# Performance work log

Hardware: AMD Instinct MI355X
Metric: run time of the kernel (lower is better)

Reference implementation:

```python
import jax, jax.numpy as jnp
import numpy as np

N, NA, F = 16384, 256, 2048
GAMMA = 1.5
BN_EPS = 1e-5


def setup_inputs() -> dict:
    key = jax.random.key(0)
    k1, k2, k3, k4, k5 = jax.random.split(key, 5)
    a = jax.random.normal(k1, (N, NA), dtype=jnp.float32)
    ps = jax.random.uniform(k2, (N, F), dtype=jnp.float32)
    lim = 1.0 / np.sqrt(NA)
    W = jax.random.uniform(k3, (F, NA), minval=-lim, maxval=lim, dtype=jnp.float32)
    b = jax.random.uniform(k4, (F,), minval=-lim, maxval=lim, dtype=jnp.float32)
    bn_w = jnp.ones((F,), dtype=jnp.float32)
    bn_b = jnp.zeros((F,), dtype=jnp.float32)
    return {"a": a, "ps": ps, "W": W, "b": b, "bn_w": bn_w, "bn_b": bn_b}


def sparsemax(z):
    # Faithful translation of the repo's Sparsemax (note: it sorts ASCENDING,
    # exactly as the original torch code does).
    D = z.shape[-1]
    s = jnp.sort(z, axis=-1)                      # ascending, [N, D]
    r = jnp.arange(D, dtype=z.dtype)              # [D]
    w = (1.0 + r * s - jnp.cumsum(s, axis=-1) > 0).astype(jnp.int32)
    k_z = jnp.max(jnp.arange(D, dtype=jnp.int32) * w, axis=-1)   # [N]
    m = (jnp.arange(D)[None, :] < (k_z + 1)[:, None]).astype(z.dtype)  # [N, D]
    m_z = jnp.sum(m * s, axis=-1)                 # [N]
    tau_z = (m_z + 1.0) / k_z.astype(z.dtype)     # [N]
    return jnp.maximum(z - tau_z[:, None], 0.0)


def reference(a, ps, W, b, bn_w, bn_b):
    # Linear: (N, n_a) -> (N, F)
    x = a @ W.T + b
    # BatchNorm1d (training mode: batch statistics, biased variance)
    mu = jnp.mean(x, axis=0)
    var = jnp.mean((x - mu) ** 2, axis=0)
    x = (x - mu) / jnp.sqrt(var + BN_EPS) * bn_w + bn_b
    # Sparsemax over prior-scaled activations
    m = sparsemax(x * ps)
    new_ps = ps * (GAMMA - jax.lax.stop_gradient(m))
    return m, new_ps
```

## Files before the change

### kernel.cpp

```cpp
#include <hip/hip_runtime.h>
#include <hip/hip_bf16.h>
#include <math.h>

#define N_ROWS 16384
#define N_A    256
#define N_F    2048
#define GAMMA  1.5f
#define BN_EPS 1e-5f

typedef __attribute__((ext_vector_type(8))) short short8;
typedef __attribute__((ext_vector_type(4))) float f32x4;

__global__ __launch_bounds__(256) void cvt_bf16(const float* __restrict__ in,
                                                unsigned short* __restrict__ out,
                                                int n4) {
    int i = blockIdx.x * 256 + threadIdx.x;
    if (i >= n4) return;
    float4 v = reinterpret_cast<const float4*>(in)[i];
    ushort4 o;
    o.x = __builtin_bit_cast(unsigned short, __float2bfloat16(v.x));
    o.y = __builtin_bit_cast(unsigned short, __float2bfloat16(v.y));
    o.z = __builtin_bit_cast(unsigned short, __float2bfloat16(v.z));
    o.w = __builtin_bit_cast(unsigned short, __float2bfloat16(v.w));
    reinterpret_cast<ushort4*>(out)[i] = o;
}

__global__ __launch_bounds__(256) void gemm_x(const unsigned short* __restrict__ aB,
                                              const unsigned short* __restrict__ wB,
                                              const float* __restrict__ bias,
                                              unsigned short* __restrict__ xB,
                                              float* __restrict__ ps1,
                                              float* __restrict__ ps2) {
    const int tid  = threadIdx.x;
    const int lane = tid & 63;
    const int wave = tid >> 6;
    const int r16  = lane & 15;
    const int quad = lane >> 4;
    const int col0 = blockIdx.x * 128;
    const int rowB = blockIdx.y * 128;
    const int row0 = rowB + wave * 32;

    __shared__ char smem[65536];

    {
        const char* wsrc = (const char*)(wB + (size_t)col0 * N_A);
        #pragma unroll
        for (int i = 0; i < 16; ++i) {
            const int c   = i * 256 + tid;
            const int row = c >> 5;
            const int off = (c & 31) * 16;
            const int src = off ^ ((row & 7) << 4);
            __builtin_amdgcn_global_load_lds(
                (const __attribute__((address_space(1))) void*)(wsrc + (size_t)row * 512 + src),
                (__attribute__((address_space(3))) void*)(smem + c * 16),
                16, 0, 0);
        }
    }

    f32x4 acc[2][8];
    #pragma unroll
    for (int g = 0; g < 2; ++g)
        #pragma unroll
        for (int t = 0; t < 8; ++t)
            acc[g][t] = (f32x4){0.f, 0.f, 0.f, 0.f};

    const unsigned short* aR0 = aB + (size_t)(row0 + r16) * N_A;
    const unsigned short* aR1 = aR0 + 16 * N_A;

    __syncthreads();

    const int swz = (r16 & 7) << 4;
    #pragma unroll
    for (int ks = 0; ks < 8; ++ks) {
        const int k0  = ks * 32 + quad * 8;
        short8 a0 = *reinterpret_cast<const short8*>(aR0 + k0);
        short8 a1 = *reinterpret_cast<const short8*>(aR1 + k0);
        const int wof = (ks * 64 + quad * 16) ^ swz;
        #pragma unroll
        for (int t = 0; t < 8; ++t) {
            short8 bf = *reinterpret_cast<const short8*>(
                            smem + (t * 16 + r16) * 512 + wof);
            acc[0][t] = __builtin_amdgcn_mfma_f32_16x16x32_bf16(a0, bf, acc[0][t], 0, 0, 0);
            acc[1][t] = __builtin_amdgcn_mfma_f32_16x16x32_bf16(a1, bf, acc[1][t], 0, 0, 0);
        }
    }

    __syncthreads();

    __shared__ float cs1[4][128];
    __shared__ float cs2[4][128];
    unsigned short (*tile)[136] = (unsigned short (*)[136])smem;

    #pragma unroll
    for (int t = 0; t < 8; ++t) {
        const float bcol = bias[col0 + t * 16 + r16];
        float s1 = 0.f, s2 = 0.f;
        #pragma unroll
        for (int g = 0; g < 2; ++g) {
            #pragma unroll
            for (int r = 0; r < 4; ++r) {
                float v = acc[g][t][r] + bcol;
                s1 += v;
                s2 += v * v;
                tile[wave * 32 + g * 16 + quad * 4 + r][t * 16 + r16] =
                    __builtin_bit_cast(unsigned short, __float2bfloat16(v));
            }
        }
        s1 += __shfl_xor(s1, 16); s1 += __shfl_xor(s1, 32);
        s2 += __shfl_xor(s2, 16); s2 += __shfl_xor(s2, 32);
        if (quad == 0) { cs1[wave][t * 16 + r16] = s1; cs2[wave][t * 16 + r16] = s2; }
    }
    __syncthreads();

    if (threadIdx.x < 128) {
        const int c = threadIdx.x;
        float s1 = cs1[0][c] + cs1[1][c] + cs1[2][c] + cs1[3][c];
        float s2 = cs2[0][c] + cs2[1][c] + cs2[2][c] + cs2[3][c];
        ps1[(size_t)blockIdx.y * N_F + col0 + c] = s1;
        ps2[(size_t)blockIdx.y * N_F + col0 + c] = s2;
    }

    {
        const int r = threadIdx.x >> 1;
        const int h = threadIdx.x & 1;
        const unsigned short* src = &tile[r][h * 64];
        unsigned short* dst = xB + (size_t)(rowB + r) * 4096 + col0 + h * 64;
        #pragma unroll
        for (int i = 0; i < 8; ++i)
            *reinterpret_cast<short8*>(dst + i * 8) =
                *reinterpret_cast<const short8*>(src + i * 8);
    }
}

__global__ __launch_bounds__(256) void finalize_stats(const float* __restrict__ ps1,
                                                      const float* __restrict__ ps2,
                                                      const float* __restrict__ bn_w,
                                                      const float* __restrict__ bn_b,
                                                      float* __restrict__ scale,
                                                      float* __restrict__ shift) {
    const int f = blockIdx.x * 256 + threadIdx.x;
    float s1 = 0.f, s2 = 0.f;
    #pragma unroll 4
    for (int i = 0; i < 128; ++i) {
        s1 += ps1[(size_t)i * N_F + f];
        s2 += ps2[(size_t)i * N_F + f];
    }
    const float inv_n = 1.0f / (float)N_ROWS;
    const float mu  = s1 * inv_n;
    const float var = s2 * inv_n - mu * mu;
    const float sc  = bn_w[f] / sqrtf(var + BN_EPS);
    scale[f] = sc;
    shift[f] = bn_b[f] - mu * sc;
}

__global__ __launch_bounds__(256) void bn_sparsemax(const unsigned short* xB,
                                                    const float* __restrict__ ps,
                                                    const float* __restrict__ scale,
                                                    const float* __restrict__ shift,
                                                    float* m_out,
                                                    float* __restrict__ ps_out) {
    const int row = blockIdx.x;
    const int tid = threadIdx.x;
    const int f0  = tid * 8;

    const unsigned short* xr = xB + (size_t)row * 4096 + f0;
    const float* pr = ps + (size_t)row * N_F + f0;

    short8 xv = *reinterpret_cast<const short8*>(xr);
    float4 p0  = *reinterpret_cast<const float4*>(pr);
    float4 p1  = *reinterpret_cast<const float4*>(pr + 4);
    float4 sc0 = *reinterpret_cast<const float4*>(scale + f0);
    float4 sc1 = *reinterpret_cast<const float4*>(scale + f0 + 4);
    float4 sh0 = *reinterpret_cast<const float4*>(shift + f0);
    float4 sh1 = *reinterpret_cast<const float4*>(shift + f0 + 4);

    float pv[8]  = {p0.x, p0.y, p0.z, p0.w, p1.x, p1.y, p1.z, p1.w};
    float scv[8] = {sc0.x, sc0.y, sc0.z, sc0.w, sc1.x, sc1.y, sc1.z, sc1.w};
    float shv[8] = {sh0.x, sh0.y, sh0.z, sh0.w, sh1.x, sh1.y, sh1.z, sh1.w};

    float z[8];
    float s = 0.f, mx = -INFINITY, mn = INFINITY;
    #pragma unroll
    for (int i = 0; i < 8; ++i) {
        float xf = __builtin_bit_cast(float,
                       (unsigned int)((unsigned short)xv[i]) << 16);
        float zz = (xf * scv[i] + shv[i]) * pv[i];
        z[i] = zz;
        s += zz;
        mx = fmaxf(mx, zz);
        mn = fminf(mn, zz);
    }

    #pragma unroll
    for (int off = 32; off > 0; off >>= 1) {
        s  += __shfl_xor(s, off);
        mx  = fmaxf(mx, __shfl_xor(mx, off));
        mn  = fminf(mn, __shfl_xor(mn, off));
    }
    __shared__ float rs[4], rmx[4], rmn[4];
    const int wave = tid >> 6;
    if ((tid & 63) == 0) { rs[wave] = s; rmx[wave] = mx; rmn[wave] = mn; }
    __syncthreads();
    s  = rs[0] + rs[1] + rs[2] + rs[3];
    mx = fmaxf(fmaxf(rmx[0], rmx[1]), fmaxf(rmx[2], rmx[3]));
    mn = fminf(fminf(rmn[0], rmn[1]), fminf(rmn[2], rmn[3]));

    const float c_last = 1.0f + (float)(N_F - 1) * mx - s;
    float tau;
    if (c_last > 0.0f) {
        tau = (s + 1.0f) / (float)(N_F - 1);
    } else {
        tau = (mn + 1.0f) / 0.0f;
    }

    float* mo = m_out  + (size_t)row * N_F + f0;
    float* po = ps_out + (size_t)row * N_F + f0;
    float4 mv0, mv1, po0, po1;
    mv0.x = fmaxf(z[0] - tau, 0.f); po0.x = pv[0] * (GAMMA - mv0.x);
    mv0.y = fmaxf(z[1] - tau, 0.f); po0.y = pv[1] * (GAMMA - mv0.y);
    mv0.z = fmaxf(z[2] - tau, 0.f); po0.z = pv[2] * (GAMMA - mv0.z);
    mv0.w = fmaxf(z[3] - tau, 0.f); po0.w = pv[3] * (GAMMA - mv0.w);
    mv1.x = fmaxf(z[4] - tau, 0.f); po1.x = pv[4] * (GAMMA - mv1.x);
    mv1.y = fmaxf(z[5] - tau, 0.f); po1.y = pv[5] * (GAMMA - mv1.y);
    mv1.z = fmaxf(z[6] - tau, 0.f); po1.z = pv[6] * (GAMMA - mv1.z);
    mv1.w = fmaxf(z[7] - tau, 0.f); po1.w = pv[7] * (GAMMA - mv1.w);
    *reinterpret_cast<float4*>(mo)     = mv0;
    *reinterpret_cast<float4*>(mo + 4) = mv1;
    *reinterpret_cast<float4*>(po)     = po0;
    *reinterpret_cast<float4*>(po + 4) = po1;
}

extern "C" void kernel_launch(void* const* d_in, const int* in_sizes, int n_in,
                              void* d_out, int out_size, void* d_ws, size_t ws_size,
                              hipStream_t stream) {
    const float* a    = (const float*)d_in[0];
    const float* ps   = (const float*)d_in[1];
    const float* W    = (const float*)d_in[2];
    const float* bias = (const float*)d_in[3];
    const float* bnw  = (const float*)d_in[4];
    const float* bnb  = (const float*)d_in[5];

    float* out    = (float*)d_out;
    float* m_out  = out;
    float* ps_out = out + (size_t)N_ROWS * N_F;
    unsigned short* xB = (unsigned short*)d_out;

    char* ws = (char*)d_ws;
    unsigned short* aB = (unsigned short*)ws;
    unsigned short* wB = (unsigned short*)(ws + (8u << 20));
    float* ps1   = (float*)(ws + (9u  << 20));
    float* ps2   = (float*)(ws + (10u << 20));
    float* scale = (float*)(ws + (11u << 20));
    float* shift = (float*)(ws + (11u << 20) + 8192);

    cvt_bf16<<<4096, 256, 0, stream>>>(a, aB, N_ROWS * N_A / 4);
    cvt_bf16<<<512, 256, 0, stream>>>(W, wB, N_F * N_A / 4);
    gemm_x<<<dim3(N_F / 128, N_ROWS / 128), 256, 0, stream>>>(aB, wB, bias, xB, ps1, ps2);
    finalize_stats<<<N_F / 256, 256, 0, stream>>>(ps1, ps2, bnw, bnb, scale, shift);
    bn_sparsemax<<<N_ROWS, 256, 0, stream>>>(xB, ps, scale, shift, m_out, ps_out);
}
```

Measured before the change: 447.6 us.

## Double-buffer GEMM K-slabs in LDS, remap blocks, one-wave-per-row sparsemax

The GEMM now stages both A and W in 64-element K slabs through LDS with double buffering, overlapping the global-to-LDS loads with MFMA work. Previously only W went through LDS and A was read straight from global memory. Block IDs are remapped so that neighbouring blocks share tiles and get better cache locality. The sparsemax kernel now gives each row to a single wave, removing the LDS reduction and __syncthreads, and it re-reads ps in the output phase rather than holding it in registers.

```diff
diff --git a/kernel.cpp b/kernel.cpp
--- a/kernel.cpp
+++ b/kernel.cpp
@@ -36,26 +36,35 @@
     const int wave = tid >> 6;
     const int r16  = lane & 15;
     const int quad = lane >> 4;
-    const int col0 = blockIdx.x * 128;
-    const int rowB = blockIdx.y * 128;
-    const int row0 = rowB + wave * 32;
+
+    const int id   = blockIdx.y * 16 + blockIdx.x;
+    const int nid  = (id & 7) * 256 + (id >> 3);
+    const int bx   = nid & 15;
+    const int by   = nid >> 4;
+    const int col0 = bx * 128;
+    const int rowB = by * 128;
 
     __shared__ char smem[65536];
-
-    {
-        const char* wsrc = (const char*)(wB + (size_t)col0 * N_A);
-        #pragma unroll
-        for (int i = 0; i < 16; ++i) {
+    char* As = smem;
+    char* Ws = smem + 32768;
+
+    auto STAGE = [&](int bo, int slab) {
+        const char* asrc = (const char*)(aB + (size_t)rowB * N_A + slab * 64);
+        const char* wsrc = (const char*)(wB + (size_t)col0 * N_A + slab * 64);
+        #pragma unroll
+        for (int i = 0; i < 4; ++i) {
             const int c   = i * 256 + tid;
-            const int row = c >> 5;
-            const int off = (c & 31) * 16;
+            const int row = c >> 3;
+            const int off = (c & 7) * 16;
             const int src = off ^ ((row & 7) << 4);
             __builtin_amdgcn_global_load_lds(
+                (const __attribute__((address_space(1))) void*)(asrc + (size_t)row * 512 + src),
+                (__attribute__((address_space(3))) void*)(As + bo + c * 16), 16, 0, 0);
+            __builtin_amdgcn_global_load_lds(
                 (const __attribute__((address_space(1))) void*)(wsrc + (size_t)row * 512 + src),
-                (__attribute__((address_space(3))) void*)(smem + c * 16),
-                16, 0, 0);
-        }
-    }
+                (__attribute__((address_space(3))) void*)(Ws + bo + c * 16), 16, 0, 0);
+        }
+    };
 
     f32x4 acc[2][8];
     #pragma unroll
@@ -64,28 +73,31 @@
         for (int t = 0; t < 8; ++t)
             acc[g][t] = (f32x4){0.f, 0.f, 0.f, 0.f};
 
-    const unsigned short* aR0 = aB + (size_t)(row0 + r16) * N_A;
-    const unsigned short* aR1 = aR0 + 16 * N_A;
-
+    STAGE(0, 0);
     __syncthreads();
 
     const int swz = (r16 & 7) << 4;
     #pragma unroll
-    for (int ks = 0; ks < 8; ++ks) {
-        const int k0  = ks * 32 + quad * 8;
-        short8 a0 = *reinterpret_cast<const short8*>(aR0 + k0);
-        short8 a1 = *reinterpret_cast<const short8*>(aR1 + k0);
-        const int wof = (ks * 64 + quad * 16) ^ swz;
-        #pragma unroll
-        for (int t = 0; t < 8; ++t) {
-            short8 bf = *reinterpret_cast<const short8*>(
-                            smem + (t * 16 + r16) * 512 + wof);
-            acc[0][t] = __builtin_amdgcn_mfma_f32_16x16x32_bf16(a0, bf, acc[0][t], 0, 0, 0);
-            acc[1][t] = __builtin_amdgcn_mfma_f32_16x16x32_bf16(a1, bf, acc[1][t], 0, 0, 0);
-        }
-    }
-
-    __syncthreads();
+    for (int s = 0; s < 4; ++s) {
+        const int bo = (s & 1) * 16384;
+        if (s < 3) STAGE(bo ^ 16384, s + 1);
+        #pragma unroll
+        for (int ks = 0; ks < 2; ++ks) {
+            const int koff = (ks * 64 + quad * 16) ^ swz;
+            short8 a0 = *reinterpret_cast<const short8*>(
+                            As + bo + (wave * 32 + r16) * 128 + koff);
+            short8 a1 = *reinterpret_cast<const short8*>(
+                            As + bo + (wave * 32 + 16 + r16) * 128 + koff);
+            #pragma unroll
+            for (int t = 0; t < 8; ++t) {
+                short8 bf = *reinterpret_cast<const short8*>(
+                                Ws + bo + (t * 16 + r16) * 128 + koff);
+                acc[0][t] = __builtin_amdgcn_mfma_f32_16x16x32_bf16(a0, bf, acc[0][t], 0, 0, 0);
+                acc[1][t] = __builtin_amdgcn_mfma_f32_16x16x32_bf16(a1, bf, acc[1][t], 0, 0, 0);
+            }
+        }
+        __syncthreads();
+    }
 
     __shared__ float cs1[4][128];
     __shared__ float cs2[4][128];
@@ -116,8 +128,8 @@
         const int c = threadIdx.x;
         float s1 = cs1[0][c] + cs1[1][c] + cs1[2][c] + cs1[3][c];
         float s2 = cs2[0][c] + cs2[1][c] + cs2[2][c] + cs2[3][c];
-        ps1[(size_t)blockIdx.y * N_F + col0 + c] = s1;
-        ps2[(size_t)blockIdx.y * N_F + col0 + c] = s2;
+        ps1[(size_t)by * N_F + col0 + c] = s1;
+        ps2[(size_t)by * N_F + col0 + c] = s2;
     }
 
     {
@@ -159,36 +171,38 @@
                                                     const float* __restrict__ shift,
                                                     float* m_out,
                                                     float* __restrict__ ps_out) {
-    const int row = blockIdx.x;
-    const int tid = threadIdx.x;
-    const int f0  = tid * 8;
-
-    const unsigned short* xr = xB + (size_t)row * 4096 + f0;
-    const float* pr = ps + (size_t)row * N_F + f0;
-
-    short8 xv = *reinterpret_cast<const short8*>(xr);
-    float4 p0  = *reinterpret_cast<const float4*>(pr);
-    float4 p1  = *reinterpret_cast<const float4*>(pr + 4);
-    float4 sc0 = *reinterpret_cast<const float4*>(scale + f0);
-    float4 sc1 = *reinterpret_cast<const float4*>(scale + f0 + 4);
-    float4 sh0 = *reinterpret_cast<const float4*>(shift + f0);
-    float4 sh1 = *reinterpret_cast<const float4*>(shift + f0 + 4);
-
-    float pv[8]  = {p0.x, p0.y, p0.z, p0.w, p1.x, p1.y, p1.z, p1.w};
-    float scv[8] = {sc0.x, sc0.y, sc0.z, sc0.w, sc1.x, sc1.y, sc1.z, sc1.w};
-    float shv[8] = {sh0.x, sh0.y, sh0.z, sh0.w, sh1.x, sh1.y, sh1.z, sh1.w};
-
-    float z[8];
+    const int wave = threadIdx.x >> 6;
+    const int lane = threadIdx.x & 63;
+    const int row  = blockIdx.x * 4 + wave;
+
+    const unsigned short* xr = xB + (size_t)row * 4096;
+    const float* pr = ps + (size_t)row * N_F;
+
+    float z[32];
     float s = 0.f, mx = -INFINITY, mn = INFINITY;
     #pragma unroll
-    for (int i = 0; i < 8; ++i) {
-        float xf = __builtin_bit_cast(float,
-                       (unsigned int)((unsigned short)xv[i]) << 16);
-        float zz = (xf * scv[i] + shv[i]) * pv[i];
-        z[i] = zz;
-        s += zz;
-        mx = fmaxf(mx, zz);
-        mn = fminf(mn, zz);
+    for (int c = 0; c < 4; ++c) {
+        const int f0 = c * 512 + lane * 8;
+        short8 xv  = *reinterpret_cast<const short8*>(xr + f0);
+        float4 p0  = *reinterpret_cast<const float4*>(pr + f0);
+        float4 p1  = *reinterpret_cast<const float4*>(pr + f0 + 4);
+        float4 sc0 = *reinterpret_cast<const float4*>(scale + f0);
+        float4 sc1 = *reinterpret_cast<const float4*>(scale + f0 + 4);
+        float4 sh0 = *reinterpret_cast<const float4*>(shift + f0);
+        float4 sh1 = *reinterpret_cast<const float4*>(shift + f0 + 4);
+        float pvc[8] = {p0.x, p0.y, p0.z, p0.w, p1.x, p1.y, p1.z, p1.w};
+        float scv[8] = {sc0.x, sc0.y, sc0.z, sc0.w, sc1.x, sc1.y, sc1.z, sc1.w};
+        float shv[8] = {sh0.x, sh0.y, sh0.z, sh0.w, sh1.x, sh1.y, sh1.z, sh1.w};
+        #pragma unroll
+        for (int i = 0; i < 8; ++i) {
+            float xf = __builtin_bit_cast(float,
+                           (unsigned int)((unsigned short)xv[i]) << 16);
+            float zz = (xf * scv[i] + shv[i]) * pvc[i];
+            z[c * 8 + i] = zz;
+            s += zz;
+            mx = fmaxf(mx, zz);
+            mn = fminf(mn, zz);
+        }
     }
 
     #pragma unroll
@@ -197,37 +211,32 @@
         mx  = fmaxf(mx, __shfl_xor(mx, off));
         mn  = fminf(mn, __shfl_xor(mn, off));
     }
-    __shared__ float rs[4], rmx[4], rmn[4];
-    const int wave = tid >> 6;
-    if ((tid & 63) == 0) { rs[wave] = s; rmx[wave] = mx; rmn[wave] = mn; }
-    __syncthreads();
-    s  = rs[0] + rs[1] + rs[2] + rs[3];
-    mx = fmaxf(fmaxf(rmx[0], rmx[1]), fmaxf(rmx[2], rmx[3]));
-    mn = fminf(fminf(rmn[0], rmn[1]), fminf(rmn[2], rmn[3]));
 
     const float c_last = 1.0f + (float)(N_F - 1) * mx - s;
-    float tau;
-    if (c_last > 0.0f) {
-        tau = (s + 1.0f) / (float)(N_F - 1);
-    } else {
-        tau = (mn + 1.0f) / 0.0f;
-    }
-
-    float* mo = m_out  + (size_t)row * N_F + f0;
-    float* po = ps_out + (size_t)row * N_F + f0;
-    float4 mv0, mv1, po0, po1;
-    mv0.x = fmaxf(z[0] - tau, 0.f); po0.x = pv[0] * (GAMMA - mv0.x);
-    mv0.y = fmaxf(z[1] - tau, 0.f); po0.y = pv[1] * (GAMMA - mv0.y);
-    mv0.z = fmaxf(z[2] - tau, 0.f); po0.z = pv[2] * (GAMMA - mv0.z);
-    mv0.w = fmaxf(z[3] - tau, 0.f); po0.w = pv[3] * (GAMMA - mv0.w);
-    mv1.x = fmaxf(z[4] - tau, 0.f); po1.x = pv[4] * (GAMMA - mv1.x);
-    mv1.y = fmaxf(z[5] - tau, 0.f); po1.y = pv[5] * (GAMMA - mv1.y);
-    mv1.z = fmaxf(z[6] - tau, 0.f); po1.z = pv[6] * (GAMMA - mv1.z);
-    mv1.w = fmaxf(z[7] - tau, 0.f); po1.w = pv[7] * (GAMMA - mv1.w);
-    *reinterpret_cast<float4*>(mo)     = mv0;
-    *reinterpret_cast<float4*>(mo + 4) = mv1;
-    *reinterpret_cast<float4*>(po)     = po0;
-    *reinterpret_cast<float4*>(po + 4) = po1;
+    const float tau = (c_last > 0.0f) ? (s + 1.0f) / (float)(N_F - 1)
+                                      : (mn + 1.0f) / 0.0f;
+
+    float* mo = m_out  + (size_t)row * N_F;
+    float* po = ps_out + (size_t)row * N_F;
+    #pragma unroll
+    for (int c = 0; c < 4; ++c) {
+        const int f0 = c * 512 + lane * 8;
+        float4 p0 = *reinterpret_cast<const float4*>(pr + f0);
+        float4 p1 = *reinterpret_cast<const float4*>(pr + f0 + 4);
+        float4 mv0, mv1, po0, po1;
+        mv0.x = fmaxf(z[c*8+0] - tau, 0.f); po0.x = p0.x * (GAMMA - mv0.x);
+        mv0.y = fmaxf(z[c*8+1] - tau, 0.f); po0.y = p0.y * (GAMMA - mv0.y);
+        mv0.z = fmaxf(z[c*8+2] - tau, 0.f); po0.z = p0.z * (GAMMA - mv0.z);
+        mv0.w = fmaxf(z[c*8+3] - tau, 0.f); po0.w = p0.w * (GAMMA - mv0.w);
+        mv1.x = fmaxf(z[c*8+4] - tau, 0.f); po1.x = p1.x * (GAMMA - mv1.x);
+        mv1.y = fmaxf(z[c*8+5] - tau, 0.f); po1.y = p1.y * (GAMMA - mv1.y);
+        mv1.z = fmaxf(z[c*8+6] - tau, 0.f); po1.z = p1.z * (GAMMA - mv1.z);
+        mv1.w = fmaxf(z[c*8+7] - tau, 0.f); po1.w = p1.w * (GAMMA - mv1.w);
+        *reinterpret_cast<float4*>(mo + f0)     = mv0;
+        *reinterpret_cast<float4*>(mo + f0 + 4) = mv1;
+        *reinterpret_cast<float4*>(po + f0)     = po0;
+        *reinterpret_cast<float4*>(po + f0 + 4) = po1;
+    }
 }
 
 extern "C" void kernel_launch(void* const* d_in, const int* in_sizes, int n_in,
@@ -257,5 +266,5 @@
     cvt_bf16<<<512, 256, 0, stream>>>(W, wB, N_F * N_A / 4);
     gemm_x<<<dim3(N_F / 128, N_ROWS / 128), 256, 0, stream>>>(aB, wB, bias, xB, ps1, ps2);
     finalize_stats<<<N_F / 256, 256, 0, stream>>>(ps1, ps2, bnw, bnb, scale, shift);
-    bn_sparsemax<<<N_ROWS, 256, 0, stream>>>(xB, ps, scale, shift, m_out, ps_out);
-}
+    bn_sparsemax<<<N_ROWS / 4, 256, 0, stream>>>(xB, ps, scale, shift, m_out, ps_out);
+}
```

After: 483.4 us. 8.0% more time.
